# Kernel tuning notes

Measured on AMD Instinct MI355X. Metric: run time of the kernel, lower is better.

The kernel has to match this reference:

```python
import jax, jax.numpy as jnp
import numpy as np
import math

B, S, E = 2, 2048, 1024
H, HD = 16, 64  # num_heads, head_size


def setup_inputs() -> dict:
    key = jax.random.key(0)
    ks = jax.random.split(key, 9)
    sc = 1.0 / math.sqrt(HD)
    return {
        "x": jax.random.normal(ks[0], (B, S, E), dtype=jnp.float32),
        "Wq_w": jax.random.normal(ks[1], (HD, HD), dtype=jnp.float32) * sc,
        "Wq_b": jax.random.normal(ks[2], (HD,), dtype=jnp.float32) * 0.02,
        "Wk_w": jax.random.normal(ks[3], (HD, HD), dtype=jnp.float32) * sc,
        "Wk_b": jax.random.normal(ks[4], (HD,), dtype=jnp.float32) * 0.02,
        "Wv_w": jax.random.normal(ks[5], (HD, HD), dtype=jnp.float32) * sc,
        "Wv_b": jax.random.normal(ks[6], (HD,), dtype=jnp.float32) * 0.02,
        "proj_w": jax.random.normal(ks[7], (E, E), dtype=jnp.float32) * (1.0 / math.sqrt(E)),
        "proj_b": jax.random.normal(ks[8], (E,), dtype=jnp.float32) * 0.02,
    }


def reference(x, Wq_w, Wq_b, Wk_w, Wk_b, Wv_w, Wv_b, proj_w, proj_b):
    b, s, _ = x.shape
    xh = x.reshape(b, s, H, HD)  # split heads; QKV linears act per-head (shared weights)
    # torch Linear: y = x @ W.T + b
    q = jnp.einsum('bshd,ed->bhse', xh, Wq_w) + Wq_b  # [B,H,S,HD]
    k = jnp.einsum('bshd,ed->bhse', xh, Wk_w) + Wk_b
    v = jnp.einsum('bshd,ed->bhse', xh, Wv_w) + Wv_b
    scores = jnp.einsum('bhqd,bhkd->bhqk', q, k) / math.sqrt(HD)
    causal = jnp.tril(jnp.ones((s, s), dtype=bool))
    scores = jnp.where(causal, scores, jnp.float32(-1e20))
    attn = jax.nn.softmax(scores, axis=-1)  # attn_dropout p=0 (eval)
    out = jnp.einsum('bhqk,bhkd->bqhd', attn, v).reshape(b, s, H * HD)
    out = out @ proj_w.T + proj_b  # resid_dropout p=0 (eval)
    return out
```

## Files before the change

### kernel.cpp

```cpp
#include <hip/hip_runtime.h>
#include <hip/hip_bf16.h>

#define B_ 2
#define S_ 2048
#define E_ 1024
#define H_ 16
#define HD_ 64
#define T_ (B_ * S_)

typedef short bf16x8 __attribute__((ext_vector_type(8)));
typedef short bf16x4 __attribute__((ext_vector_type(4)));
typedef float f32x4 __attribute__((ext_vector_type(4)));

__device__ __forceinline__ short f2bf(float f) {
  union { float f; unsigned u; } v;
  v.f = f;
  unsigned r = v.u + 0x7fffu + ((v.u >> 16) & 1u);
  return (short)(r >> 16);
}


__global__ __launch_bounds__(256) void qkv_conv_kernel(
    const float* __restrict__ x,
    const float* __restrict__ wq, const float* __restrict__ bq,
    const float* __restrict__ wk, const float* __restrict__ bk,
    const float* __restrict__ wv, const float* __restrict__ bv,
    short* __restrict__ Q, short* __restrict__ KV,
    const float* __restrict__ pw, short* __restrict__ pwb) {
  const int tid = threadIdx.x;
  if (blockIdx.x >= 512) {
    int i = ((blockIdx.x - 512) * 256 + tid) * 4;
    float4 f = *(const float4*)(pw + i);
    bf16x4 o;
    o[0] = f2bf(f.x); o[1] = f2bf(f.y); o[2] = f2bf(f.z); o[3] = f2bf(f.w);
    *(bf16x4*)(pwb + i) = o;
    return;
  }
  __shared__ short Xs[64][136];
  __shared__ short Ws[192][72];
  __shared__ short Qt[64][68], Kt[64][68], Vt[64][68];

  const int bid = blockIdx.x;
  const int tb = bid >> 3, hg = bid & 7;
  const int s0 = (tb * 64) & (S_ - 1);
  const int kt = s0 >> 6;
  const int bb = (tb * 64) >> 11;
  const int wave = tid >> 6, lane = tid & 63;
  const int lrow = lane & 15, quad = lane >> 4;

#pragma unroll
  for (int i = 0; i < 8; i++) {
    int c = tid + 256 * i;
    int row = c >> 5, col4 = c & 31;
    float4 f = *(const float4*)(x + ((long)(tb * 64 + row)) * E_ + hg * 128 + col4 * 4);
    bf16x4 o;
    o[0] = f2bf(f.x); o[1] = f2bf(f.y); o[2] = f2bf(f.z); o[3] = f2bf(f.w);
    *(bf16x4*)&Xs[row][col4 * 4] = o;
  }
#pragma unroll
  for (int m = 0; m < 3; m++) {
    const float* w = (m == 0) ? wq : (m == 1) ? wk : wv;
#pragma unroll
    for (int i = 0; i < 4; i++) {
      int c = tid + 256 * i;
      int row = m * 64 + (c >> 4), col = (c & 15) * 4;
      float4 f = *(const float4*)(w + (long)c * 4);
      bf16x4 o;
      o[0] = f2bf(f.x); o[1] = f2bf(f.y); o[2] = f2bf(f.z); o[3] = f2bf(f.w);
      *(bf16x4*)&Ws[row][col] = o;
    }
  }
  float bias[12];
#pragma unroll
  for (int nb = 0; nb < 12; nb++) {
    int sel = nb >> 2;
    int e = ((nb & 3) * 16) + lrow;
    bias[nb] = ((sel == 0) ? bq : (sel == 1) ? bk : bv)[e];
  }
  __syncthreads();

  bf16x8 bf0[12], bf1[12];
#pragma unroll
  for (int nb = 0; nb < 12; nb++) {
    bf0[nb] = *(bf16x8*)&Ws[nb * 16 + lrow][quad * 8];
    bf1[nb] = *(bf16x8*)&Ws[nb * 16 + lrow][32 + quad * 8];
  }

  const float QSCALE = 0.125f * 1.44269504089f;
  for (int hl = 0; hl < 2; hl++) {
    const int h = hg * 2 + hl;
    bf16x8 a0 = *(bf16x8*)&Xs[wave * 16 + lrow][hl * 64 + quad * 8];
    bf16x8 a1 = *(bf16x8*)&Xs[wave * 16 + lrow][hl * 64 + 32 + quad * 8];
#pragma unroll
    for (int nb = 0; nb < 12; nb++) {
      f32x4 acc = {0.f, 0.f, 0.f, 0.f};
      acc = __builtin_amdgcn_mfma_f32_16x16x32_bf16(a0, bf0[nb], acc, 0, 0, 0);
      acc = __builtin_amdgcn_mfma_f32_16x16x32_bf16(a1, bf1[nb], acc, 0, 0, 0);
      const int sel = nb >> 2;
      const float scale = (sel == 0) ? QSCALE : 1.0f;
      short (*ct)[68] = (sel == 0) ? Qt : (sel == 1) ? Kt : Vt;
#pragma unroll
      for (int r = 0; r < 4; r++) {
        ct[wave * 16 + quad * 4 + r][(nb & 3) * 16 + lrow] =
            f2bf((acc[r] + bias[nb]) * scale);
      }
    }
    __syncthreads();

    const int bh = bb * H_ + h;
    short* Qg = Q + ((long)bh * S_ + s0) * HD_;
    short* Tg = KV + ((long)(bh * 32 + kt)) * 8192;
#pragma unroll
    for (int i = 0; i < 2; i++) {
      int c = tid + 256 * i;
      int row = c >> 3, col = (c & 7) * 8;
      *(bf16x8*)(Qg + (long)row * HD_ + col) = *(bf16x8*)&Qt[row][col];
    }
#pragma unroll
    for (int u = 0; u < 4; u++) {
      int fid = tid + 256 * u;
      bf16x8 val;
      int lane2 = fid & 63;
      int quad2 = lane2 >> 4, lrow2 = lane2 & 15;
      if (u < 2) {
        int g = fid >> 6;
        int nb = g >> 1, half = g & 1;
        val = *(bf16x8*)&Kt[nb * 16 + lrow2][half * 32 + quad2 * 8];
      } else {
        int g = (fid >> 6) & 7;
        int p2 = g >> 2, db = g & 3;
#pragma unroll
        for (int j = 0; j < 8; j++) {
          int key = (2 * p2 + (j >> 2)) * 16 + quad2 * 4 + (j & 3);
          val[j] = Vt[key][db * 16 + lrow2];
        }
      }
      *(bf16x8*)(Tg + fid * 8) = val;
    }
    __syncthreads();
  }
}

__global__ __launch_bounds__(256, 2) void attn_kernel(
    const short* __restrict__ Q, const short* __restrict__ KV,
    short* __restrict__ O ) {
  __shared__ short L[2][8192];

  const int tid = threadIdx.x;
  const int bid = blockIdx.x;
  const int bh = bid & 31;
  const int pr = bid >> 5;
  const int g = (pr < 8) ? (15 - pr) : (pr - 8);
  const int b = bh >> 4, h = bh & 15;
  const long qbase = ((long)bh) << 17;

  const int wave = tid >> 6, lane = tid & 63;
  const int lrow = lane & 15, quad = lane >> 4;
  const int qgA = g * 128 + wave * 16 + lrow;
  const int qgB = qgA + 64;

  const short* qpA = Q + qbase + (long)qgA * HD_;
  const short* qpB = Q + qbase + (long)qgB * HD_;
  bf16x8 qfA0 = *(const bf16x8*)(qpA + quad * 8);
  bf16x8 qfA1 = *(const bf16x8*)(qpA + 32 + quad * 8);
  bf16x8 qfB0 = *(const bf16x8*)(qpB + quad * 8);
  bf16x8 qfB1 = *(const bf16x8*)(qpB + 32 + quad * 8);

  const short* Tg = KV + ((long)bh * 32) * 8192 + tid * 8;
  bf16x8 reg[4];
  auto LD = [&](int kt) {
    const short* p = Tg + (long)kt * 8192;
#pragma unroll
    for (int u = 0; u < 4; u++) reg[u] = *(const bf16x8*)(p + u * 2048);
  };

  f32x4 OA[4], OB[4];
#pragma unroll
  for (int db = 0; db < 4; db++) {
    OA[db] = f32x4{0.f, 0.f, 0.f, 0.f};
    OB[db] = f32x4{0.f, 0.f, 0.f, 0.f};
  }
  float lsA = 0.f, lsB = 0.f;

  const int nkt = 2 * g + 2;
  LD(0);
  for (int kt = 0; kt < nkt; kt++) {
    const int buf = kt & 1;
#pragma unroll
    for (int u = 0; u < 4; u++)
      *(bf16x8*)&L[buf][(tid + 256 * u) * 8] = reg[u];
    __syncthreads();
    if (kt + 1 < nkt) LD(kt + 1);

    bf16x8 kf[8];
#pragma unroll
    for (int g2 = 0; g2 < 8; g2++)
      kf[g2] = *(bf16x8*)&L[buf][g2 * 512 + lane * 8];

    const bool doA = (kt < nkt - 1);

    f32x4 scA[4], scB[4];
#pragma unroll
    for (int nb = 0; nb < 4; nb++) {
      f32x4 cb = {0.f, 0.f, 0.f, 0.f};
      cb = __builtin_amdgcn_mfma_f32_16x16x32_bf16(kf[2 * nb], qfB0, cb, 0, 0, 0);
      cb = __builtin_amdgcn_mfma_f32_16x16x32_bf16(kf[2 * nb + 1], qfB1, cb, 0, 0, 0);
      scB[nb] = cb;
    }
    if (doA) {
#pragma unroll
      for (int nb = 0; nb < 4; nb++) {
        f32x4 ca = {0.f, 0.f, 0.f, 0.f};
        ca = __builtin_amdgcn_mfma_f32_16x16x32_bf16(kf[2 * nb], qfA0, ca, 0, 0, 0);
        ca = __builtin_amdgcn_mfma_f32_16x16x32_bf16(kf[2 * nb + 1], qfA1, ca, 0, 0, 0);
        scA[nb] = ca;
      }
    }

    bf16x8 vf[8];
#pragma unroll
    for (int g2 = 0; g2 < 8; g2++)
      vf[g2] = *(bf16x8*)&L[buf][4096 + g2 * 512 + lane * 8];

    if (kt == nkt - 2) {
      const int k0 = kt * 64;
#pragma unroll
      for (int nb = 0; nb < 4; nb++) {
        int kgl = k0 + nb * 16 + quad * 4;
#pragma unroll
        for (int r = 0; r < 4; r++)
          if (kgl + r > qgA) scA[nb][r] = -1e30f;
      }
    }
    if (kt == nkt - 1) {
      const int k0 = kt * 64;
#pragma unroll
      for (int nb = 0; nb < 4; nb++) {
        int kgl = k0 + nb * 16 + quad * 4;
#pragma unroll
        for (int r = 0; r < 4; r++)
          if (kgl + r > qgB) scB[nb][r] = -1e30f;
      }
    }

    bf16x4 pfA[4], pfB[4];
#pragma unroll
    for (int nb = 0; nb < 4; nb++) {
      unsigned ub[4];
#pragma unroll
      for (int r = 0; r < 4; r++) {
        float p = __builtin_amdgcn_exp2f(scB[nb][r]);
        lsB += p;
        ub[r] = __float_as_uint(p);
      }
      union { unsigned q[2]; bf16x4 v; } pk;
      pk.q[0] = __builtin_amdgcn_perm(ub[1], ub[0], 0x07060302u);
      pk.q[1] = __builtin_amdgcn_perm(ub[3], ub[2], 0x07060302u);
      pfB[nb] = pk.v;
    }
    if (doA) {
#pragma unroll
      for (int nb = 0; nb < 4; nb++) {
        unsigned ua[4];
#pragma unroll
        for (int r = 0; r < 4; r++) {
          float p = __builtin_amdgcn_exp2f(scA[nb][r]);
          lsA += p;
          ua[r] = __float_as_uint(p);
        }
        union { unsigned q[2]; bf16x4 v; } pk;
        pk.q[0] = __builtin_amdgcn_perm(ua[1], ua[0], 0x07060302u);
        pk.q[1] = __builtin_amdgcn_perm(ua[3], ua[2], 0x07060302u);
        pfA[nb] = pk.v;
      }
    }

#pragma unroll
    for (int p2 = 0; p2 < 2; p2++) {
#pragma unroll
      for (int db = 0; db < 4; db++) {
        bf16x8 vv = vf[p2 * 4 + db];
        bf16x4 vlo = {vv[0], vv[1], vv[2], vv[3]};
        bf16x4 vhi = {vv[4], vv[5], vv[6], vv[7]};
        OB[db] = __builtin_amdgcn_mfma_f32_16x16x16bf16_1k(vlo, pfB[2 * p2], OB[db], 0, 0, 0);
        OB[db] = __builtin_amdgcn_mfma_f32_16x16x16bf16_1k(vhi, pfB[2 * p2 + 1], OB[db], 0, 0, 0);
        if (doA) {
          OA[db] = __builtin_amdgcn_mfma_f32_16x16x16bf16_1k(vlo, pfA[2 * p2], OA[db], 0, 0, 0);
          OA[db] = __builtin_amdgcn_mfma_f32_16x16x16bf16_1k(vhi, pfA[2 * p2 + 1], OA[db], 0, 0, 0);
        }
      }
    }
  }

  lsA += __shfl_xor(lsA, 16);
  lsA += __shfl_xor(lsA, 32);
  lsB += __shfl_xor(lsB, 16);
  lsB += __shfl_xor(lsB, 32);
  const float invA = 1.f / lsA, invB = 1.f / lsB;
  short* oA = O + ((long)b * S_ + qgA) * E_ + h * HD_;
  short* oB = O + ((long)b * S_ + qgB) * E_ + h * HD_;
#pragma unroll
  for (int db = 0; db < 4; db++) {
    bf16x4 oa, ob;
#pragma unroll
    for (int r = 0; r < 4; r++) {
      oa[r] = f2bf(OA[db][r] * invA);
      ob[r] = f2bf(OB[db][r] * invB);
    }
    *(bf16x4*)(oA + db * 16 + quad * 4) = oa;
    *(bf16x4*)(oB + db * 16 + quad * 4) = ob;
  }
}

__global__ __launch_bounds__(256) void proj_kernel(
    const short* __restrict__ A, const short* __restrict__ W,
    const float* __restrict__ bias, float* __restrict__ out) {
  __shared__ short As[2][128][40];
  __shared__ short Bs[2][64][40];
  const int tid = threadIdx.x;
  const int bid = blockIdx.x;
  const int m0 = (bid >> 4) * 128;
  const int n0 = (bid & 15) * 64;
  const int wave = tid >> 6, lane = tid & 63;
  const int wm = wave >> 1, wn = wave & 1;
  const int lrow = lane & 15, quad = lane >> 4;

  const int ar = tid >> 1, ac = (tid & 1) * 16;
  const int br = tid >> 2, bc = (tid & 3) * 8;

  bf16x8 a0, a1, b0;
  auto LDR = [&](int k0) {
    const short* ap = A + (long)(m0 + ar) * E_ + k0 + ac;
    a0 = *(const bf16x8*)(ap);
    a1 = *(const bf16x8*)(ap + 8);
    b0 = *(const bf16x8*)(W + (long)(n0 + br) * E_ + k0 + bc);
  };

  f32x4 acc[4][2];
#pragma unroll
  for (int i = 0; i < 4; i++)
#pragma unroll
    for (int j = 0; j < 2; j++) acc[i][j] = f32x4{0.f, 0.f, 0.f, 0.f};

  LDR(0);
  for (int kk = 0; kk < 32; kk++) {
    const int buf = kk & 1;
    *(bf16x8*)&As[buf][ar][ac] = a0;
    *(bf16x8*)&As[buf][ar][ac + 8] = a1;
    *(bf16x8*)&Bs[buf][br][bc] = b0;
    __syncthreads();
    if (kk < 31) LDR((kk + 1) * 32);

    bf16x8 af[4], bfr[2];
#pragma unroll
    for (int i = 0; i < 4; i++)
      af[i] = *(bf16x8*)&As[buf][wm * 64 + i * 16 + lrow][quad * 8];
#pragma unroll
    for (int j = 0; j < 2; j++)
      bfr[j] = *(bf16x8*)&Bs[buf][wn * 32 + j * 16 + lrow][quad * 8];
#pragma unroll
    for (int i = 0; i < 4; i++)
#pragma unroll
      for (int j = 0; j < 2; j++)
        acc[i][j] = __builtin_amdgcn_mfma_f32_16x16x32_bf16(af[i], bfr[j], acc[i][j], 0, 0, 0);
  }

#pragma unroll
  for (int j = 0; j < 2; j++) {
    int col = n0 + wn * 32 + j * 16 + lrow;
    float bv = bias[col];
#pragma unroll
    for (int i = 0; i < 4; i++) {
#pragma unroll
      for (int r = 0; r < 4; r++) {
        int row = m0 + wm * 64 + i * 16 + quad * 4 + r;
        out[(long)row * E_ + col] = acc[i][j][r] + bv;
      }
    }
  }
}

extern "C" void kernel_launch(void* const* d_in, const int* in_sizes, int n_in,
                              void* d_out, int out_size, void* d_ws, size_t ws_size,
                              hipStream_t stream) {
  const float* x  = (const float*)d_in[0];
  const float* wq = (const float*)d_in[1];
  const float* bq = (const float*)d_in[2];
  const float* wk = (const float*)d_in[3];
  const float* bk = (const float*)d_in[4];
  const float* wv = (const float*)d_in[5];
  const float* bv = (const float*)d_in[6];
  const float* pw = (const float*)d_in[7];
  const float* pb = (const float*)d_in[8];
  float* out = (float*)d_out;

  char* ws = (char*)d_ws;
  short* Qb = (short*)(ws);
  short* KVb = (short*)(ws + (size_t)8 * 1024 * 1024);
  short* AO = (short*)(ws + (size_t)24 * 1024 * 1024);
  short* PW = (short*)(ws + (size_t)32 * 1024 * 1024);

  qkv_conv_kernel<<<dim3(512 + 1024), dim3(256), 0, stream>>>(
      x, wq, bq, wk, bk, wv, bv, Qb, KVb, pw, PW);
  attn_kernel<<<dim3(16 * 32), dim3(256), 0, stream>>>(Qb, KVb, AO);
  proj_kernel<<<dim3(32 * 16), dim3(256), 0, stream>>>(AO, PW, pb, out);
}
```

Measured before the change: 140.3 us.

## Stage attention KV via direct global-to-LDS loads with doubled tiles; deepen proj K-step

The attention kernel now uses global_load_lds to copy 128-key super-tiles straight into shared memory, skipping the register round trip. It processes two 64-key subtiles per barrier, which halves the number of syncs, and doubles LDS to 64KB per block. The projection GEMM widens its K step from 32 to 64 with more loads per thread and half as many loop iterations. The larger LDS footprint may reduce occupancy, and the causal mask and last-tile handling had to be re-indexed for the new tile shape.

```diff
diff --git a/kernel.cpp b/kernel.cpp
--- a/kernel.cpp
+++ b/kernel.cpp
@@ -17,6 +17,12 @@
   v.f = f;
   unsigned r = v.u + 0x7fffu + ((v.u >> 16) & 1u);
   return (short)(r >> 16);
+}
+
+__device__ __forceinline__ void gll16(const void* g, void* l) {
+  __builtin_amdgcn_global_load_lds(
+      (const __attribute__((address_space(1))) unsigned int*)g,
+      (__attribute__((address_space(3))) unsigned int*)l, 16, 0, 0);
 }
 
 
@@ -144,7 +150,7 @@
 __global__ __launch_bounds__(256, 2) void attn_kernel(
     const short* __restrict__ Q, const short* __restrict__ KV,
     short* __restrict__ O ) {
-  __shared__ short L[2][8192];
+  __shared__ __align__(16) short L[2][16384];
 
   const int tid = threadIdx.x;
   const int bid = blockIdx.x;
@@ -166,12 +172,15 @@
   bf16x8 qfB0 = *(const bf16x8*)(qpB + quad * 8);
   bf16x8 qfB1 = *(const bf16x8*)(qpB + 32 + quad * 8);
 
-  const short* Tg = KV + ((long)bh * 32) * 8192 + tid * 8;
-  bf16x8 reg[4];
-  auto LD = [&](int kt) {
-    const short* p = Tg + (long)kt * 8192;
-#pragma unroll
-    for (int u = 0; u < 4; u++) reg[u] = *(const bf16x8*)(p + u * 2048);
+  const char* Tg = (const char*)(KV + ((long)bh * 32) * 8192);
+
+  auto STAGE = [&](int sup, int buf) {
+    const char* gt = Tg + (long)sup * 32768;
+#pragma unroll
+    for (int u = 0; u < 8; u++) {
+      const int chunk = u * 4 + wave;
+      gll16(gt + chunk * 1024 + lane * 16, &L[buf][chunk * 512]);
+    }
   };
 
   f32x4 OA[4], OB[4];
@@ -182,111 +191,113 @@
   }
   float lsA = 0.f, lsB = 0.f;
 
-  const int nkt = 2 * g + 2;
-  LD(0);
-  for (int kt = 0; kt < nkt; kt++) {
-    const int buf = kt & 1;
-#pragma unroll
-    for (int u = 0; u < 4; u++)
-      *(bf16x8*)&L[buf][(tid + 256 * u) * 8] = reg[u];
+  const int nsup = g + 1;
+  STAGE(0, 0);
+  for (int it = 0; it < nsup; it++) {
+    const int buf = it & 1;
     __syncthreads();
-    if (kt + 1 < nkt) LD(kt + 1);
-
-    bf16x8 kf[8];
-#pragma unroll
-    for (int g2 = 0; g2 < 8; g2++)
-      kf[g2] = *(bf16x8*)&L[buf][g2 * 512 + lane * 8];
-
-    const bool doA = (kt < nkt - 1);
-
-    f32x4 scA[4], scB[4];
-#pragma unroll
-    for (int nb = 0; nb < 4; nb++) {
-      f32x4 cb = {0.f, 0.f, 0.f, 0.f};
-      cb = __builtin_amdgcn_mfma_f32_16x16x32_bf16(kf[2 * nb], qfB0, cb, 0, 0, 0);
-      cb = __builtin_amdgcn_mfma_f32_16x16x32_bf16(kf[2 * nb + 1], qfB1, cb, 0, 0, 0);
-      scB[nb] = cb;
-    }
-    if (doA) {
+    if (it + 1 < nsup) STAGE(it + 1, buf ^ 1);
+    const bool last = (it == nsup - 1);
+
+#pragma unroll
+    for (int s2 = 0; s2 < 2; s2++) {
+      const short* Lb = &L[buf][s2 * 8192];
+      const bool doA = !(last && s2 == 1);
+
+      bf16x8 kf[8];
+#pragma unroll
+      for (int g2 = 0; g2 < 8; g2++)
+        kf[g2] = *(bf16x8*)&Lb[g2 * 512 + lane * 8];
+
+      f32x4 scA[4], scB[4];
 #pragma unroll
       for (int nb = 0; nb < 4; nb++) {
-        f32x4 ca = {0.f, 0.f, 0.f, 0.f};
-        ca = __builtin_amdgcn_mfma_f32_16x16x32_bf16(kf[2 * nb], qfA0, ca, 0, 0, 0);
-        ca = __builtin_amdgcn_mfma_f32_16x16x32_bf16(kf[2 * nb + 1], qfA1, ca, 0, 0, 0);
-        scA[nb] = ca;
-      }
-    }
-
-    bf16x8 vf[8];
-#pragma unroll
-    for (int g2 = 0; g2 < 8; g2++)
-      vf[g2] = *(bf16x8*)&L[buf][4096 + g2 * 512 + lane * 8];
-
-    if (kt == nkt - 2) {
-      const int k0 = kt * 64;
+        f32x4 cb = {0.f, 0.f, 0.f, 0.f};
+        cb = __builtin_amdgcn_mfma_f32_16x16x32_bf16(kf[2 * nb], qfB0, cb, 0, 0, 0);
+        cb = __builtin_amdgcn_mfma_f32_16x16x32_bf16(kf[2 * nb + 1], qfB1, cb, 0, 0, 0);
+        scB[nb] = cb;
+      }
+      if (doA) {
+#pragma unroll
+        for (int nb = 0; nb < 4; nb++) {
+          f32x4 ca = {0.f, 0.f, 0.f, 0.f};
+          ca = __builtin_amdgcn_mfma_f32_16x16x32_bf16(kf[2 * nb], qfA0, ca, 0, 0, 0);
+          ca = __builtin_amdgcn_mfma_f32_16x16x32_bf16(kf[2 * nb + 1], qfA1, ca, 0, 0, 0);
+          scA[nb] = ca;
+        }
+      }
+
+      bf16x8 vf[8];
+#pragma unroll
+      for (int g2 = 0; g2 < 8; g2++)
+        vf[g2] = *(bf16x8*)&Lb[4096 + g2 * 512 + lane * 8];
+
+      if (last && s2 == 0) {
+        const int k0 = 2 * g * 64;
+#pragma unroll
+        for (int nb = 0; nb < 4; nb++) {
+          int kgl = k0 + nb * 16 + quad * 4;
+#pragma unroll
+          for (int r = 0; r < 4; r++)
+            if (kgl + r > qgA) scA[nb][r] = -1e30f;
+        }
+      }
+      if (last && s2 == 1) {
+        const int k0 = (2 * g + 1) * 64;
+#pragma unroll
+        for (int nb = 0; nb < 4; nb++) {
+          int kgl = k0 + nb * 16 + quad * 4;
+#pragma unroll
+          for (int r = 0; r < 4; r++)
+            if (kgl + r > qgB) scB[nb][r] = -1e30f;
+        }
+      }
+
+      bf16x4 pfA[4], pfB[4];
 #pragma unroll
       for (int nb = 0; nb < 4; nb++) {
-        int kgl = k0 + nb * 16 + quad * 4;
-#pragma unroll
-        for (int r = 0; r < 4; r++)
-          if (kgl + r > qgA) scA[nb][r] = -1e30f;
-      }
-    }
-    if (kt == nkt - 1) {
-      const int k0 = kt * 64;
-#pragma unroll
-      for (int nb = 0; nb < 4; nb++) {
-        int kgl = k0 + nb * 16 + quad * 4;
-#pragma unroll
-        for (int r = 0; r < 4; r++)
-          if (kgl + r > qgB) scB[nb][r] = -1e30f;
-      }
-    }
-
-    bf16x4 pfA[4], pfB[4];
-#pragma unroll
-    for (int nb = 0; nb < 4; nb++) {
-      unsigned ub[4];
-#pragma unroll
-      for (int r = 0; r < 4; r++) {
-        float p = __builtin_amdgcn_exp2f(scB[nb][r]);
-        lsB += p;
-        ub[r] = __float_as_uint(p);
-      }
-      union { unsigned q[2]; bf16x4 v; } pk;
-      pk.q[0] = __builtin_amdgcn_perm(ub[1], ub[0], 0x07060302u);
-      pk.q[1] = __builtin_amdgcn_perm(ub[3], ub[2], 0x07060302u);
-      pfB[nb] = pk.v;
-    }
-    if (doA) {
-#pragma unroll
-      for (int nb = 0; nb < 4; nb++) {
-        unsigned ua[4];
+        unsigned ub[4];
 #pragma unroll
         for (int r = 0; r < 4; r++) {
-          float p = __builtin_amdgcn_exp2f(scA[nb][r]);
-          lsA += p;
-          ua[r] = __float_as_uint(p);
+          float p = __builtin_amdgcn_exp2f(scB[nb][r]);
+          lsB += p;
+          ub[r] = __float_as_uint(p);
         }
         union { unsigned q[2]; bf16x4 v; } pk;
-        pk.q[0] = __builtin_amdgcn_perm(ua[1], ua[0], 0x07060302u);
-        pk.q[1] = __builtin_amdgcn_perm(ua[3], ua[2], 0x07060302u);
-        pfA[nb] = pk.v;
-      }
-    }
-
-#pragma unroll
-    for (int p2 = 0; p2 < 2; p2++) {
-#pragma unroll
-      for (int db = 0; db < 4; db++) {
-        bf16x8 vv = vf[p2 * 4 + db];
-        bf16x4 vlo = {vv[0], vv[1], vv[2], vv[3]};
-        bf16x4 vhi = {vv[4], vv[5], vv[6], vv[7]};
-        OB[db] = __builtin_amdgcn_mfma_f32_16x16x16bf16_1k(vlo, pfB[2 * p2], OB[db], 0, 0, 0);
-        OB[db] = __builtin_amdgcn_mfma_f32_16x16x16bf16_1k(vhi, pfB[2 * p2 + 1], OB[db], 0, 0, 0);
-        if (doA) {
-          OA[db] = __builtin_amdgcn_mfma_f32_16x16x16bf16_1k(vlo, pfA[2 * p2], OA[db], 0, 0, 0);
-          OA[db] = __builtin_amdgcn_mfma_f32_16x16x16bf16_1k(vhi, pfA[2 * p2 + 1], OA[db], 0, 0, 0);
+        pk.q[0] = __builtin_amdgcn_perm(ub[1], ub[0], 0x07060302u);
+        pk.q[1] = __builtin_amdgcn_perm(ub[3], ub[2], 0x07060302u);
+        pfB[nb] = pk.v;
+      }
+      if (doA) {
+#pragma unroll
+        for (int nb = 0; nb < 4; nb++) {
+          unsigned ua[4];
+#pragma unroll
+          for (int r = 0; r < 4; r++) {
+            float p = __builtin_amdgcn_exp2f(scA[nb][r]);
+            lsA += p;
+            ua[r] = __float_as_uint(p);
+          }
+          union { unsigned q[2]; bf16x4 v; } pk;
+          pk.q[0] = __builtin_amdgcn_perm(ua[1], ua[0], 0x07060302u);
+          pk.q[1] = __builtin_amdgcn_perm(ua[3], ua[2], 0x07060302u);
+          pfA[nb] = pk.v;
+        }
+      }
+
+#pragma unroll
+      for (int p2 = 0; p2 < 2; p2++) {
+#pragma unroll
+        for (int db = 0; db < 4; db++) {
+          bf16x8 vv = vf[p2 * 4 + db];
+          bf16x4 vlo = {vv[0], vv[1], vv[2], vv[3]};
+          bf16x4 vhi = {vv[4], vv[5], vv[6], vv[7]};
+          OB[db] = __builtin_amdgcn_mfma_f32_16x16x16bf16_1k(vlo, pfB[2 * p2], OB[db], 0, 0, 0);
+          OB[db] = __builtin_amdgcn_mfma_f32_16x16x16bf16_1k(vhi, pfB[2 * p2 + 1], OB[db], 0, 0, 0);
+          if (doA) {
+            OA[db] = __builtin_amdgcn_mfma_f32_16x16x16bf16_1k(vlo, pfA[2 * p2], OA[db], 0, 0, 0);
+            OA[db] = __builtin_amdgcn_mfma_f32_16x16x16bf16_1k(vhi, pfA[2 * p2 + 1], OA[db], 0, 0, 0);
+          }
         }
       }
     }
@@ -315,8 +326,8 @@
 __global__ __launch_bounds__(256) void proj_kernel(
     const short* __restrict__ A, const short* __restrict__ W,
     const float* __restrict__ bias, float* __restrict__ out) {
-  __shared__ short As[2][128][40];
-  __shared__ short Bs[2][64][40];
+  __shared__ short As[2][128][72];
+  __shared__ short Bs[2][64][72];
   const int tid = threadIdx.x;
   const int bid = blockIdx.x;
   const int m0 = (bid >> 4) * 128;
@@ -325,15 +336,22 @@
   const int wm = wave >> 1, wn = wave & 1;
   const int lrow = lane & 15, quad = lane >> 4;
 
-  const int ar = tid >> 1, ac = (tid & 1) * 16;
-  const int br = tid >> 2, bc = (tid & 3) * 8;
-
-  bf16x8 a0, a1, b0;
+  const int sr = tid >> 3, sc = (tid & 7) * 8;
+
+  bf16x8 ar[4], br[2];
   auto LDR = [&](int k0) {
-    const short* ap = A + (long)(m0 + ar) * E_ + k0 + ac;
-    a0 = *(const bf16x8*)(ap);
-    a1 = *(const bf16x8*)(ap + 8);
-    b0 = *(const bf16x8*)(W + (long)(n0 + br) * E_ + k0 + bc);
+#pragma unroll
+    for (int u = 0; u < 4; u++) {
+      int cid = tid + 256 * u;
+      int row = cid >> 3, col = (cid & 7) * 8;
+      ar[u] = *(const bf16x8*)(A + (long)(m0 + row) * E_ + k0 + col);
+    }
+#pragma unroll
+    for (int u = 0; u < 2; u++) {
+      int cid = tid + 256 * u;
+      int row = cid >> 3, col = (cid & 7) * 8;
+      br[u] = *(const bf16x8*)(W + (long)(n0 + row) * E_ + k0 + col);
+    }
   };
 
   f32x4 acc[4][2];
@@ -343,26 +361,36 @@
     for (int j = 0; j < 2; j++) acc[i][j] = f32x4{0.f, 0.f, 0.f, 0.f};
 
   LDR(0);
-  for (int kk = 0; kk < 32; kk++) {
+  for (int kk = 0; kk < 16; kk++) {
     const int buf = kk & 1;
-    *(bf16x8*)&As[buf][ar][ac] = a0;
-    *(bf16x8*)&As[buf][ar][ac + 8] = a1;
-    *(bf16x8*)&Bs[buf][br][bc] = b0;
+#pragma unroll
+    for (int u = 0; u < 4; u++) {
+      int cid = tid + 256 * u;
+      *(bf16x8*)&As[buf][cid >> 3][(cid & 7) * 8] = ar[u];
+    }
+#pragma unroll
+    for (int u = 0; u < 2; u++) {
+      int cid = tid + 256 * u;
+      *(bf16x8*)&Bs[buf][cid >> 3][(cid & 7) * 8] = br[u];
+    }
     __syncthreads();
-    if (kk < 31) LDR((kk + 1) * 32);
-
-    bf16x8 af[4], bfr[2];
-#pragma unroll
-    for (int i = 0; i < 4; i++)
-      af[i] = *(bf16x8*)&As[buf][wm * 64 + i * 16 + lrow][quad * 8];
-#pragma unroll
-    for (int j = 0; j < 2; j++)
-      bfr[j] = *(bf16x8*)&Bs[buf][wn * 32 + j * 16 + lrow][quad * 8];
-#pragma unroll
-    for (int i = 0; i < 4; i++)
+    if (kk < 15) LDR((kk + 1) * 64);
+
+#pragma unroll
+    for (int kh = 0; kh < 2; kh++) {
+      bf16x8 af[4], bfr[2];
+#pragma unroll
+      for (int i = 0; i < 4; i++)
+        af[i] = *(bf16x8*)&As[buf][wm * 64 + i * 16 + lrow][kh * 32 + quad * 8];
 #pragma unroll
       for (int j = 0; j < 2; j++)
-        acc[i][j] = __builtin_amdgcn_mfma_f32_16x16x32_bf16(af[i], bfr[j], acc[i][j], 0, 0, 0);
+        bfr[j] = *(bf16x8*)&Bs[buf][wn * 32 + j * 16 + lrow][kh * 32 + quad * 8];
+#pragma unroll
+      for (int i = 0; i < 4; i++)
+#pragma unroll
+        for (int j = 0; j < 2; j++)
+          acc[i][j] = __builtin_amdgcn_mfma_f32_16x16x32_bf16(af[i], bfr[j], acc[i][j], 0, 0, 0);
+    }
   }
 
 #pragma unroll
```

After: 135.2 us. 3.7% less time.
